# Performance work log

Hardware: AMD Instinct MI355X
Metric: run time of the kernel (lower is better)

Reference implementation:

```python
import jax, jax.numpy as jnp
import numpy as np

EPS = 1e-5
TOP_K = 3
W_THRESH = 0.01

def _bn(x, g, b):
    # training-mode batch norm over (N,H,W) per channel
    m = x.mean(axis=(0, 2, 3), keepdims=True)
    v = x.var(axis=(0, 2, 3), keepdims=True)
    return (x - m) * jax.lax.rsqrt(v + EPS) * g[None, :, None, None] + b[None, :, None, None]

def _conv(x, w, stride=1, pad=0, dil=1, groups=1):
    return jax.lax.conv_general_dilated(
        x, w, (stride, stride), [(pad, pad), (pad, pad)],
        rhs_dilation=(dil, dil),
        dimension_numbers=("NCHW", "OIHW", "NCHW"),
        feature_group_count=groups)

def _maxpool3(x):
    return jax.lax.reduce_window(x, -jnp.inf, jax.lax.max, (1, 1, 3, 3), (1, 1, 1, 1),
                                 [(0, 0), (0, 0), (1, 1), (1, 1)])

def _avgpool3(x):
    s = jax.lax.reduce_window(x, 0.0, jax.lax.add, (1, 1, 3, 3), (1, 1, 1, 1),
                              [(0, 0), (0, 0), (1, 1), (1, 1)])
    return s / 9.0  # count_include_pad=True as in torch avg_pool2d

def setup_inputs() -> dict:
    key = jax.random.key(0)
    ks = jax.random.split(key, 16)
    Cin, C = 128, 256
    B, H, W = 64, 32, 32
    f = lambda k, shp, s=0.05: jax.random.normal(k, shp, dtype=jnp.float32) * s
    gamma = lambda k, n: 1.0 + 0.1 * jax.random.normal(k, (n,), dtype=jnp.float32)
    return {
        "x": jax.random.normal(ks[0], (B, Cin, H, W), dtype=jnp.float32),
        "arch_weights": jax.random.normal(ks[1], (8,), dtype=jnp.float32),
        "w_in": f(ks[2], (C, Cin, 1, 1)),
        "g_in": gamma(ks[3], C), "b_in": jnp.zeros((C,), jnp.float32),
        "w3": f(ks[4], (C, C, 3, 3)),
        "g3": gamma(ks[5], C), "b3": jnp.zeros((C,), jnp.float32),
        "w5": f(ks[6], (C, C, 5, 5)),
        "g5": gamma(ks[7], C), "b5": jnp.zeros((C,), jnp.float32),
        "w_dw": f(ks[8], (C, 1, 3, 3), 0.2),
        "w_pw": f(ks[9], (C, C, 1, 1)),
        "gs": gamma(ks[10], C), "bs": jnp.zeros((C,), jnp.float32),
        "wd": f(ks[11], (C, C, 3, 3)),
        "gd": gamma(ks[12], C), "bd": jnp.zeros((C,), jnp.float32),
        "gmp": gamma(ks[13], C), "bmp": jnp.zeros((C,), jnp.float32),
        "gap": gamma(ks[14], C), "bap": jnp.zeros((C,), jnp.float32),
    }

def _forward(x, arch_weights, w_in, g_in, b_in, w3, g3, b3, w5, g5, b5,
             w_dw, w_pw, gs, bs, wd, gd, bd, gmp, bmp, gap, bap):
    # input transition: 1x1 conv -> BN -> ReLU (in_channels != out_channels)
    h = jax.nn.relu(_bn(_conv(x, w_in), g_in, b_in))
    # top-k thresholded renormalized mixture weights over 8 candidate ops
    w = jax.nn.softmax(arch_weights)
    tv, ti = jax.lax.top_k(w, TOP_K)
    sel = jnp.zeros_like(w).at[ti].set(tv)
    sel = jnp.where(sel >= W_THRESH, sel, 0.0)
    sel = sel / jnp.maximum(sel.sum(), 1e-12)
    r = jax.nn.relu(h)
    # op order: [none, max_pool_3x3, avg_pool_3x3, skip, conv_3x3, conv_5x5, sep_conv_3x3, dil_conv_3x3]
    out = sel[1] * _bn(_maxpool3(h), gmp, bmp)
    out = out + sel[2] * _bn(_avgpool3(h), gap, bap)
    out = out + sel[3] * h
    out = out + sel[4] * _bn(_conv(r, w3, pad=1), g3, b3)
    out = out + sel[5] * _bn(_conv(r, w5, pad=2), g5, b5)
    out = out + sel[6] * _bn(_conv(_conv(r, w_dw, pad=1, groups=r.shape[1]), w_pw), gs, bs)
    out = out + sel[7] * _bn(_conv(r, wd, pad=2, dil=2), gd, bd)
    return out

def reference(x, arch_weights, w_in, g_in, b_in, w3, g3, b3, w5, g5, b5,
              w_dw, w_pw, gs, bs, wd, gd, bd, gmp, bmp, gap, bap):
    return _forward(x, arch_weights, w_in, g_in, b_in, w3, g3, b3, w5, g5, b5,
                    w_dw, w_pw, gs, bs, wd, gd, bd, gmp, bmp, gap, bap)
```

## Files before the change

kernel.cpp:

```cpp
#include <hip/hip_runtime.h>

#define CIN_  128
#define C_    256
#define HW_   1024
#define NPC_  65536.0f
#define NB_   16384

constexpr size_t NELEM = 16777216ull;

__device__ float g_sel[8];
__device__ float g_stats[8 * 512];
__device__ int   g_isf32;
__device__ float g_h[NELEM];
__device__ float g_c3[NELEM];
__device__ float g_c5[NELEM];
__device__ float g_cd[NELEM];
__device__ float g_pm[NELEM];
__device__ float g_pa[NELEM];
__device__ float g_pw[NELEM];
__device__ float g_dw[NELEM];

__device__ float g_w5f[32 * 256 * 25 * 8];
__device__ float g_w3f[32 * 256 * 9 * 8];
__device__ float g_wdf[32 * 256 * 9 * 8];
__device__ float g_wtf[32 * 128 * 8];

__device__ __forceinline__ float u2f(unsigned short u) {
    union { unsigned int i; float f; } x; x.i = ((unsigned int)u) << 16; return x.f;
}
__device__ __forceinline__ unsigned short f2u(float f) {
    union { float f; unsigned int i; } x; x.f = f;
    unsigned int r = x.i + 0x7fffu + ((x.i >> 16) & 1u);
    return (unsigned short)(r >> 16);
}
__device__ __forceinline__ float ldq(const void* p, long i, int isf32) {
    return isf32 ? ((const float*)p)[i] : u2f(((const unsigned short*)p)[i]);
}

__global__ void k_prep(const void* __restrict__ x, const void* __restrict__ aw) {
    __shared__ int flag_s;
    __shared__ float red[256];
    const int t = threadIdx.x;
    for (int i = t; i < 8 * 512; i += 256) g_stats[i] = 0.f;
    const unsigned short* xu = (const unsigned short*)x;
    int bad = 0;
    for (int i = t; i < 8192; i += 256) {
        unsigned int e = (xu[i] >> 7) & 0xFFu;
        if (e >= 0xC6u) ++bad;
    }
    red[t] = (float)bad;
    __syncthreads();
    for (int off = 128; off > 0; off >>= 1) {
        if (t < off) red[t] += red[t + off];
        __syncthreads();
    }
    if (t == 0) { flag_s = (red[0] > 4.0f) ? 1 : 0; g_isf32 = flag_s; }
    __syncthreads();
    const int isf32 = flag_s;
    if (t == 0) {
        float w[8];
        float mx = -1e30f;
        for (int i = 0; i < 8; ++i) { w[i] = ldq(aw, i, isf32); mx = fmaxf(mx, w[i]); }
        float s = 0.f;
        for (int i = 0; i < 8; ++i) { w[i] = expf(w[i] - mx); s += w[i]; }
        for (int i = 0; i < 8; ++i) w[i] /= s;
        float sv[8] = {0,0,0,0,0,0,0,0};
        bool used[8] = {false,false,false,false,false,false,false,false};
        for (int k = 0; k < 3; ++k) {
            int bi = -1; float bv = -1.f;
            for (int i = 0; i < 8; ++i) if (!used[i] && w[i] > bv) { bv = w[i]; bi = i; }
            used[bi] = true; sv[bi] = bv;
        }
        float tot = 0.f;
        for (int i = 0; i < 8; ++i) { if (sv[i] < 0.01f) sv[i] = 0.f; tot += sv[i]; }
        tot = fmaxf(tot, 1e-12f);
        for (int i = 0; i < 8; ++i) g_sel[i] = sv[i] / tot;
    }
}

__global__ __launch_bounds__(256)
void k_wconv(const void* __restrict__ w3, const void* __restrict__ w5,
             const void* __restrict__ wd, const void* __restrict__ wi) {
    const int cg = blockIdx.x;
    const int t  = threadIdx.x;
    const int isf32 = g_isf32;
    for (int o = t; o < 51200; o += 256) {
        int u = o & 7, r = o >> 3, tap = r % 25, ci = r / 25;
        g_w5f[(size_t)cg * 51200 + o] =
            ldq(w5, ((long)(cg * 8 + u) * C_ + ci) * 25 + tap, isf32);
    }
    for (int o = t; o < 18432; o += 256) {
        int u = o & 7, r = o >> 3, tap = r % 9, ci = r / 9;
        long ii = ((long)(cg * 8 + u) * C_ + ci) * 9 + tap;
        g_w3f[(size_t)cg * 18432 + o] = ldq(w3, ii, isf32);
        g_wdf[(size_t)cg * 18432 + o] = ldq(wd, ii, isf32);
    }
    for (int o = t; o < 1024; o += 256) {
        int u = o & 7, ci = o >> 3;
        g_wtf[cg * 1024 + o] = ldq(wi, (long)(cg * 8 + u) * CIN_ + ci, isf32);
    }
}

__device__ __forceinline__ void stats_epilogue(float* red, float s, float s2,
                                               int t, int c, int slot) {
    __syncthreads();
    red[t] = s; red[t + 256] = s2;
    __syncthreads();
    for (int off = 128; off > 0; off >>= 1) {
        if (t < off) { red[t] += red[t + off]; red[t + 256] += red[t + 256 + off]; }
        __syncthreads();
    }
    if (t == 0) {
        atomicAdd(&g_stats[slot * 512 + c], red[0]);
        atomicAdd(&g_stats[slot * 512 + 256 + c], red[256]);
    }
}

__device__ __forceinline__ void stats_ep2(float* red, int t,
                                          float sA, float s2A, float sB, float s2B,
                                          int cA, int cB, int slot) {
    __syncthreads();
    red[t] = sA; red[t + 256] = s2A; red[t + 512] = sB; red[t + 768] = s2B;
    __syncthreads();
    for (int off = 128; off > 0; off >>= 1) {
        if (t < off) {
            red[t]       += red[t + off];
            red[t + 256] += red[t + 256 + off];
            red[t + 512] += red[t + 512 + off];
            red[t + 768] += red[t + 768 + off];
        }
        __syncthreads();
    }
    if (t == 0) {
        atomicAdd(&g_stats[slot * 512 + cA],       red[0]);
        atomicAdd(&g_stats[slot * 512 + 256 + cA], red[256]);
        atomicAdd(&g_stats[slot * 512 + cB],       red[512]);
        atomicAdd(&g_stats[slot * 512 + 256 + cB], red[768]);
    }
}

__global__ __launch_bounds__(256)
void k_trans(const void* __restrict__ xin) {
    __shared__ float xs[2][HW_];
    __shared__ float red[1024];
    const int t  = threadIdx.x;
    const int cg = blockIdx.x & 31;
    const int c0 = cg * 8;
    const int b  = blockIdx.x >> 5;
    const int isf32 = g_isf32;
    const float* wb = g_wtf + cg * 1024;
    float acc[8][4];
    #pragma unroll
    for (int k = 0; k < 8; ++k)
        #pragma unroll
        for (int j = 0; j < 4; ++j) acc[k][j] = 0.f;

    {
        size_t vi = (size_t)(b * CIN_) * 256 + t;
        float4 r0;
        if (isf32) r0 = ((const float4*)xin)[vi];
        else {
            ushort4 r = ((const ushort4*)xin)[vi];
            r0.x = u2f(r.x); r0.y = u2f(r.y); r0.z = u2f(r.z); r0.w = u2f(r.w);
        }
        xs[0][t*4+0] = r0.x; xs[0][t*4+1] = r0.y;
        xs[0][t*4+2] = r0.z; xs[0][t*4+3] = r0.w;
    }
    __syncthreads();
    int cur = 0;
    for (int ci = 0; ci < CIN_; ++ci) {
        float4 rN = {0.f, 0.f, 0.f, 0.f};
        if (ci + 1 < CIN_) {
            size_t vi = (size_t)(b * CIN_ + ci + 1) * 256 + t;
            if (isf32) rN = ((const float4*)xin)[vi];
            else {
                ushort4 r = ((const ushort4*)xin)[vi];
                rN.x = u2f(r.x); rN.y = u2f(r.y); rN.z = u2f(r.z); rN.w = u2f(r.w);
            }
        }
        const float x0v = xs[cur][t      ], x1v = xs[cur][t + 256];
        const float x2v = xs[cur][t + 512], x3v = xs[cur][t + 768];
        float4 wq0 = *(const float4*)(wb + ci * 8);
        float4 wq1 = *(const float4*)(wb + ci * 8 + 4);
        acc[0][0] += x0v*wq0.x; acc[0][1] += x1v*wq0.x; acc[0][2] += x2v*wq0.x; acc[0][3] += x3v*wq0.x;
        acc[1][0] += x0v*wq0.y; acc[1][1] += x1v*wq0.y; acc[1][2] += x2v*wq0.y; acc[1][3] += x3v*wq0.y;
        acc[2][0] += x0v*wq0.z; acc[2][1] += x1v*wq0.z; acc[2][2] += x2v*wq0.z; acc[2][3] += x3v*wq0.z;
        acc[3][0] += x0v*wq0.w; acc[3][1] += x1v*wq0.w; acc[3][2] += x2v*wq0.w; acc[3][3] += x3v*wq0.w;
        acc[4][0] += x0v*wq1.x; acc[4][1] += x1v*wq1.x; acc[4][2] += x2v*wq1.x; acc[4][3] += x3v*wq1.x;
        acc[5][0] += x0v*wq1.y; acc[5][1] += x1v*wq1.y; acc[5][2] += x2v*wq1.y; acc[5][3] += x3v*wq1.y;
        acc[6][0] += x0v*wq1.z; acc[6][1] += x1v*wq1.z; acc[6][2] += x2v*wq1.z; acc[6][3] += x3v*wq1.z;
        acc[7][0] += x0v*wq1.w; acc[7][1] += x1v*wq1.w; acc[7][2] += x2v*wq1.w; acc[7][3] += x3v*wq1.w;
        if (ci + 1 < CIN_) {
            float* xw = xs[cur ^ 1] + t * 4;
            xw[0] = rN.x; xw[1] = rN.y; xw[2] = rN.z; xw[3] = rN.w;
        }
        __syncthreads();
        cur ^= 1;
    }
    #pragma unroll
    for (int k = 0; k < 8; ++k) {
        float* o = g_dw + (size_t)(b * C_ + c0 + k) * HW_;
        o[t] = acc[k][0]; o[t + 256] = acc[k][1];
        o[t + 512] = acc[k][2]; o[t + 768] = acc[k][3];
    }
    #pragma unroll
    for (int k = 0; k < 8; k += 2) {
        float sA  = acc[k][0] + acc[k][1] + acc[k][2] + acc[k][3];
        float s2A = acc[k][0]*acc[k][0] + acc[k][1]*acc[k][1]
                  + acc[k][2]*acc[k][2] + acc[k][3]*acc[k][3];
        float sB  = acc[k+1][0] + acc[k+1][1] + acc[k+1][2] + acc[k+1][3];
        float s2B = acc[k+1][0]*acc[k+1][0] + acc[k+1][1]*acc[k+1][1]
                  + acc[k+1][2]*acc[k+1][2] + acc[k+1][3]*acc[k+1][3];
        stats_ep2(red, t, sA, s2A, sB, s2B, c0 + k, c0 + k + 1, 0);
    }
}

__global__ __launch_bounds__(256)
void k_bnrelu(const void* __restrict__ g, const void* __restrict__ bb) {
    size_t idx = ((size_t)blockIdx.x * 256 + threadIdx.x) * 4;
    int c = (int)((idx >> 10) & (C_ - 1));
    int isf32 = g_isf32;
    float mean = g_stats[c] * (1.0f / NPC_);
    float var  = g_stats[256 + c] * (1.0f / NPC_) - mean * mean;
    float rstd = rsqrtf(fmaxf(var, 0.f) + 1e-5f);
    float gv = ldq(g, c, isf32), bv = ldq(bb, c, isf32);
    float4 r = *(const float4*)(g_dw + idx);
    float4 h;
    h.x = fmaxf(0.f, (r.x - mean) * rstd * gv + bv);
    h.y = fmaxf(0.f, (r.y - mean) * rstd * gv + bv);
    h.z = fmaxf(0.f, (r.z - mean) * rstd * gv + bv);
    h.w = fmaxf(0.f, (r.w - mean) * rstd * gv + bv);
    *(float4*)(g_h + idx) = h;
}

__global__ __launch_bounds__(256)
void k_pool_fused() {
    const float s1 = g_sel[1], s2 = g_sel[2];
    if (s1 == 0.f && s2 == 0.f) return;
    __shared__ float xs[34 * 33];
    __shared__ float red[512];
    const int t = threadIdx.x;
    const int c = blockIdx.x & (C_ - 1);
    const int y  = t >> 3;
    const int x0 = (t & 7) * 4;
    const float* hp = g_h + (size_t)blockIdx.x * HW_;
    float4 r = *(const float4*)(hp + t * 4);
    float* xw = xs + y * 33 + x0;
    xw[0] = r.x; xw[1] = r.y; xw[2] = r.z; xw[3] = r.w;
    __syncthreads();
    float mx[4] = {0.f, 0.f, 0.f, 0.f};
    float sm[4] = {0.f, 0.f, 0.f, 0.f};
    #pragma unroll
    for (int ky = 0; ky < 3; ++ky) {
        int iy = y + ky - 1;
        if (iy < 0 || iy >= 32) continue;
        float row[6];
        #pragma unroll
        for (int i = 0; i < 6; ++i) {
            int ix = x0 + i - 1;
            row[i] = (ix >= 0 && ix < 32) ? xs[iy * 33 + ix] : 0.0f;
        }
        #pragma unroll
        for (int kx = 0; kx < 3; ++kx)
            #pragma unroll
            for (int j = 0; j < 4; ++j) {
                mx[j] = fmaxf(mx[j], row[j + kx]);
                sm[j] += row[j + kx];
            }
    }
    #pragma unroll
    for (int j = 0; j < 4; ++j) sm[j] *= (1.0f / 9.0f);
    const size_t ob = (size_t)blockIdx.x * HW_ + y * 32 + x0;
    if (s1 != 0.f) {
        float* o = g_pm + ob;
        o[0] = mx[0]; o[1] = mx[1]; o[2] = mx[2]; o[3] = mx[3];
        stats_epilogue(red, mx[0]+mx[1]+mx[2]+mx[3],
                       mx[0]*mx[0]+mx[1]*mx[1]+mx[2]*mx[2]+mx[3]*mx[3], t, c, 1);
    }
    if (s2 != 0.f) {
        float* o = g_pa + ob;
        o[0] = sm[0]; o[1] = sm[1]; o[2] = sm[2]; o[3] = sm[3];
        stats_epilogue(red, sm[0]+sm[1]+sm[2]+sm[3],
                       sm[0]*sm[0]+sm[1]*sm[1]+sm[2]*sm[2]+sm[3]*sm[3], t, c, 2);
    }
}

template<int KS, int DIL, int PAD, int SLOT>
__global__ __launch_bounds__(256)
void k_conv1() {
    if (g_sel[SLOT] == 0.0f) return;
    constexpr int TR   = 32 + 2 * PAD;
    constexpr int TAPS = KS * KS;
    __shared__ float xs[2][TR * 40];
    __shared__ float red[1024];
    const int t  = threadIdx.x;
    const int cg = blockIdx.x & 31;
    const int c0 = cg * 8;
    const int b  = blockIdx.x >> 5;
    const int y  = t >> 3;
    const int x0 = (t & 7) * 4;
    const float* hb = g_h + (size_t)b * C_ * HW_;
    const float* wb = (SLOT == 4 ? g_w3f : SLOT == 5 ? g_w5f : g_wdf)
                      + (size_t)cg * (C_ * TAPS * 8);
    float* obuf = (SLOT == 4) ? g_c3 : (SLOT == 5) ? g_c5 : g_cd;

    float acc[8][4];
    #pragma unroll
    for (int u = 0; u < 8; ++u)
        #pragma unroll
        for (int j = 0; j < 4; ++j) acc[u][j] = 0.f;

    {
        float* xf = &xs[0][0];
        for (int i = t; i < 2 * TR * 40; i += 256) xf[i] = 0.f;
    }
    __syncthreads();
    {
        float4 r0 = *(const float4*)(hb + t * 4);
        *(float4*)(xs[0] + (y + PAD) * 40 + 4 + x0) = r0;
    }
    __syncthreads();
    int cur = 0;

    for (int ci = 0; ci < C_; ++ci) {
        float4 rN = {0.f, 0.f, 0.f, 0.f};
        if (ci + 1 < C_)
            rN = *(const float4*)(hb + (size_t)(ci + 1) * HW_ + t * 4);
        const float* xsc = xs[cur];
        const float* wc  = wb + ci * (TAPS * 8);
        #pragma unroll
        for (int ky = 0; ky < KS; ++ky) {
            const int rr = (y + ky * DIL) * 40 + x0;
            float wnd[12];
            if (PAD == 1) {
                wnd[3] = xsc[rr + 3];
                float4 qb = *(const float4*)(xsc + rr + 4);
                wnd[4] = qb.x; wnd[5] = qb.y; wnd[6] = qb.z; wnd[7] = qb.w;
                wnd[8] = xsc[rr + 8];
            } else {
                float2 qa = *(const float2*)(xsc + rr + 2);
                float4 qb = *(const float4*)(xsc + rr + 4);
                float2 qc = *(const float2*)(xsc + rr + 8);
                wnd[2] = qa.x; wnd[3] = qa.y;
                wnd[4] = qb.x; wnd[5] = qb.y; wnd[6] = qb.z; wnd[7] = qb.w;
                wnd[8] = qc.x; wnd[9] = qc.y;
            }
            #pragma unroll
            for (int kx = 0; kx < KS; ++kx) {
                const float4 wA = *(const float4*)(wc + (ky * KS + kx) * 8);
                const float4 wB = *(const float4*)(wc + (ky * KS + kx) * 8 + 4);
                #pragma unroll
                for (int j = 0; j < 4; ++j) {
                    const float v = wnd[(4 - PAD) + j + kx * DIL];
                    acc[0][j] += v * wA.x; acc[1][j] += v * wA.y;
                    acc[2][j] += v * wA.z; acc[3][j] += v * wA.w;
                    acc[4][j] += v * wB.x; acc[5][j] += v * wB.y;
                    acc[6][j] += v * wB.z; acc[7][j] += v * wB.w;
                }
            }
        }
        if (ci + 1 < C_)
            *(float4*)(xs[cur ^ 1] + (y + PAD) * 40 + 4 + x0) = rN;
        __syncthreads();
        cur ^= 1;
    }

    #pragma unroll
    for (int u = 0; u < 8; ++u) {
        float4 o; o.x = acc[u][0]; o.y = acc[u][1]; o.z = acc[u][2]; o.w = acc[u][3];
        *(float4*)(obuf + (size_t)(b * C_ + c0 + u) * HW_ + y * 32 + x0) = o;
    }
    #pragma unroll
    for (int u = 0; u < 8; u += 2)
        stats_ep2(red, t,
            acc[u][0]+acc[u][1]+acc[u][2]+acc[u][3],
            acc[u][0]*acc[u][0]+acc[u][1]*acc[u][1]+acc[u][2]*acc[u][2]+acc[u][3]*acc[u][3],
            acc[u+1][0]+acc[u+1][1]+acc[u+1][2]+acc[u+1][3],
            acc[u+1][0]*acc[u+1][0]+acc[u+1][1]*acc[u+1][1]+acc[u+1][2]*acc[u+1][2]+acc[u+1][3]*acc[u+1][3],
            c0 + u, c0 + u + 1, SLOT);
}

__global__ __launch_bounds__(256)
void k_dw(const void* __restrict__ wt) {
    if (g_sel[6] == 0.0f) return;
    __shared__ float xs[34 * 33];
    const int t = threadIdx.x;
    const int c = blockIdx.x & (C_ - 1);
    const int y  = t >> 3;
    const int x0 = (t & 7) * 4;
    const int isf32 = g_isf32;
    const float* hp = g_h + (size_t)blockIdx.x * HW_;
    float4 r = *(const float4*)(hp + t * 4);
    float* xw = xs + y * 33 + x0;
    xw[0] = r.x; xw[1] = r.y; xw[2] = r.z; xw[3] = r.w;
    __syncthreads();
    float wv[9];
    #pragma unroll
    for (int k = 0; k < 9; ++k) wv[k] = ldq(wt, (long)c * 9 + k, isf32);
    float acc[4] = {0.f, 0.f, 0.f, 0.f};
    #pragma unroll
    for (int ky = 0; ky < 3; ++ky) {
        int iy = y + ky - 1;
        if (iy < 0 || iy >= 32) continue;
        float row[6];
        #pragma unroll
        for (int i = 0; i < 6; ++i) {
            int ix = x0 + i - 1;
            row[i] = (ix >= 0 && ix < 32) ? xs[iy * 33 + ix] : 0.0f;
        }
        #pragma unroll
        for (int kx = 0; kx < 3; ++kx)
            #pragma unroll
            for (int j = 0; j < 4; ++j)
                acc[j] += row[j + kx] * wv[ky * 3 + kx];
    }
    float* o = g_dw + (size_t)blockIdx.x * HW_ + y * 32 + x0;
    o[0] = acc[0]; o[1] = acc[1]; o[2] = acc[2]; o[3] = acc[3];
}

__global__ __launch_bounds__(256)
void k_pw(const void* __restrict__ wt) {
    if (g_sel[6] == 0.0f) return;
    __shared__ float xs[HW_];
    __shared__ float red[1024];
    const int t = threadIdx.x;
    const int c0 = (blockIdx.x & 31) * 8;
    const int b  = blockIdx.x >> 5;
    const int isf32 = g_isf32;
    const float* hb = g_dw + (size_t)b * C_ * HW_;
    float acc[8][4];
    #pragma unroll
    for (int k = 0; k < 8; ++k)
        #pragma unroll
        for (int j = 0; j < 4; ++j) acc[k][j] = 0.f;
    for (int ci = 0; ci < C_; ++ci) {
        __syncthreads();
        float4 r = *(const float4*)(hb + (size_t)ci * HW_ + t * 4);
        xs[t*4+0] = r.x; xs[t*4+1] = r.y; xs[t*4+2] = r.z; xs[t*4+3] = r.w;
        __syncthreads();
        const float x0v = xs[t], x1v = xs[t + 256], x2v = xs[t + 512], x3v = xs[t + 768];
        #pragma unroll
        for (int k = 0; k < 8; ++k) {
            float wv = ldq(wt, (long)(c0 + k) * C_ + ci, isf32);
            acc[k][0] += x0v * wv; acc[k][1] += x1v * wv;
            acc[k][2] += x2v * wv; acc[k][3] += x3v * wv;
        }
    }
    #pragma unroll
    for (int k = 0; k < 8; ++k) {
        float* o = g_pw + (size_t)(b * C_ + c0 + k) * HW_;
        o[t] = acc[k][0]; o[t + 256] = acc[k][1];
        o[t + 512] = acc[k][2]; o[t + 768] = acc[k][3];
    }
    #pragma unroll
    for (int k = 0; k < 8; k += 2) {
        float sA  = acc[k][0] + acc[k][1] + acc[k][2] + acc[k][3];
        float s2A = acc[k][0]*acc[k][0] + acc[k][1]*acc[k][1]
                  + acc[k][2]*acc[k][2] + acc[k][3]*acc[k][3];
        float sB  = acc[k+1][0] + acc[k+1][1] + acc[k+1][2] + acc[k+1][3];
        float s2B = acc[k+1][0]*acc[k+1][0] + acc[k+1][1]*acc[k+1][1]
                  + acc[k+1][2]*acc[k+1][2] + acc[k+1][3]*acc[k+1][3];
        stats_ep2(red, t, sA, s2A, sB, s2B, c0 + k, c0 + k + 1, 6);
    }
}

__device__ __forceinline__ void bn_term(float4& o, const float* buf, size_t idx,
                                        int c, int slot, float sv,
                                        const void* g, const void* bb, int isf32) {
    float mean = g_stats[slot * 512 + c] * (1.0f / NPC_);
    float var  = g_stats[slot * 512 + 256 + c] * (1.0f / NPC_) - mean * mean;
    float rstd = rsqrtf(fmaxf(var, 0.f) + 1e-5f);
    float gv = ldq(g, c, isf32), bv = ldq(bb, c, isf32);
    float4 r = *(const float4*)(buf + idx);
    o.x += sv * ((r.x - mean) * rstd * gv + bv);
    o.y += sv * ((r.y - mean) * rstd * gv + bv);
    o.z += sv * ((r.z - mean) * rstd * gv + bv);
    o.w += sv * ((r.w - mean) * rstd * gv + bv);
}

__global__ __launch_bounds__(256)
void k_final_all(void* __restrict__ out,
                 const void* __restrict__ gmp, const void* __restrict__ bmp,
                 const void* __restrict__ gap, const void* __restrict__ bap,
                 const void* __restrict__ g3,  const void* __restrict__ b3,
                 const void* __restrict__ g5,  const void* __restrict__ b5,
                 const void* __restrict__ gs,  const void* __restrict__ bs,
                 const void* __restrict__ gd,  const void* __restrict__ bd) {
    size_t idx = ((size_t)blockIdx.x * 256 + threadIdx.x) * 4;
    int c = (int)((idx >> 10) & (C_ - 1));
    int isf32 = g_isf32;
    float4 o = {0.f, 0.f, 0.f, 0.f};
    float s3 = g_sel[3];
    if (s3 != 0.f) {
        float4 h = *(const float4*)(g_h + idx);
        o.x = s3 * h.x; o.y = s3 * h.y; o.z = s3 * h.z; o.w = s3 * h.w;
    }
    float sv;
    if ((sv = g_sel[1]) != 0.f) bn_term(o, g_pm, idx, c, 1, sv, gmp, bmp, isf32);
    if ((sv = g_sel[2]) != 0.f) bn_term(o, g_pa, idx, c, 2, sv, gap, bap, isf32);
    if ((sv = g_sel[4]) != 0.f) bn_term(o, g_c3, idx, c, 4, sv, g3,  b3,  isf32);
    if ((sv = g_sel[5]) != 0.f) bn_term(o, g_c5, idx, c, 5, sv, g5,  b5,  isf32);
    if ((sv = g_sel[6]) != 0.f) bn_term(o, g_pw, idx, c, 6, sv, gs,  bs,  isf32);
    if ((sv = g_sel[7]) != 0.f) bn_term(o, g_cd, idx, c, 7, sv, gd,  bd,  isf32);
    if (isf32) {
        *(float4*)((float*)out + idx) = o;
    } else {
        ushort4 u; u.x = f2u(o.x); u.y = f2u(o.y); u.z = f2u(o.z); u.w = f2u(o.w);
        *(ushort4*)((unsigned short*)out + idx) = u;
    }
}

extern "C" void kernel_launch(void* const* d_in, const int* in_sizes, int n_in,
                              void* d_out, int out_size, void* d_ws, size_t ws_size,
                              hipStream_t stream) {
    const void* x    = d_in[0];
    const void* aw   = d_in[1];
    const void* w_in = d_in[2];
    const void* g_in = d_in[3];
    const void* b_in = d_in[4];
    const void* w3   = d_in[5];
    const void* g3   = d_in[6];
    const void* b3   = d_in[7];
    const void* w5   = d_in[8];
    const void* g5   = d_in[9];
    const void* b5   = d_in[10];
    const void* wdw  = d_in[11];
    const void* wpw  = d_in[12];
    const void* gs   = d_in[13];
    const void* bs   = d_in[14];
    const void* wd   = d_in[15];
    const void* gd   = d_in[16];
    const void* bd   = d_in[17];
    const void* gmp  = d_in[18];
    const void* bmp  = d_in[19];
    const void* gap  = d_in[20];
    const void* bap  = d_in[21];

    dim3 Bk(256);
    dim3 Gfull(NB_);
    dim3 Gc8(2048);

    k_prep<<<dim3(1), Bk, 0, stream>>>(x, aw);
    k_wconv<<<dim3(32), Bk, 0, stream>>>(w3, w5, wd, w_in);

    k_trans<<<Gc8, Bk, 0, stream>>>(x);
    k_bnrelu<<<Gfull, Bk, 0, stream>>>(g_in, b_in);

    k_pool_fused<<<Gfull, Bk, 0, stream>>>();

    k_conv1<3, 1, 1, 4><<<Gc8, Bk, 0, stream>>>();
    k_conv1<5, 1, 2, 5><<<Gc8, Bk, 0, stream>>>();
    k_conv1<3, 2, 2, 7><<<Gc8, Bk, 0, stream>>>();

    k_dw<<<Gfull, Bk, 0, stream>>>(wdw);
    k_pw<<<Gc8, Bk, 0, stream>>>(wpw);

    k_final_all<<<Gfull, Bk, 0, stream>>>(d_out,
        gmp, bmp, gap, bap, g3, b3, g5, b5, gs, bs, gd, bd);
}
```

Before: 1.219 ms.

## Make conv tiles per-wavefront and drop block barriers in 1x1 convs

The spatial conv kernels now give each 64-lane wavefront its own 8-row tile with its own double-buffered shared-memory halo. This removes the per-input-channel __syncthreads, at the cost of redundant halo loads and larger per-block LDS. The 1x1 input and pointwise convs read activations straight from global memory instead of staging through shared memory with barriers. The pointwise weights are pre-transposed into a channel-interleaved float buffer for vectorized loads. Stats reduction is factored into a helper.

```diff
diff --git a/kernel.cpp b/kernel.cpp
--- a/kernel.cpp
+++ b/kernel.cpp
@@ -24,6 +24,7 @@
 __device__ float g_w3f[32 * 256 * 9 * 8];
 __device__ float g_wdf[32 * 256 * 9 * 8];
 __device__ float g_wtf[32 * 128 * 8];
+__device__ float g_wpf[32 * 256 * 8];
 
 __device__ __forceinline__ float u2f(unsigned short u) {
     union { unsigned int i; float f; } x; x.i = ((unsigned int)u) << 16; return x.f;
@@ -36,6 +37,16 @@
 __device__ __forceinline__ float ldq(const void* p, long i, int isf32) {
     return isf32 ? ((const float*)p)[i] : u2f(((const unsigned short*)p)[i]);
 }
+
+#define FMA8X4(acc, wq0, wq1, x0v, x1v, x2v, x3v)                                     \
+    acc[0][0] += x0v*wq0.x; acc[0][1] += x1v*wq0.x; acc[0][2] += x2v*wq0.x; acc[0][3] += x3v*wq0.x; \
+    acc[1][0] += x0v*wq0.y; acc[1][1] += x1v*wq0.y; acc[1][2] += x2v*wq0.y; acc[1][3] += x3v*wq0.y; \
+    acc[2][0] += x0v*wq0.z; acc[2][1] += x1v*wq0.z; acc[2][2] += x2v*wq0.z; acc[2][3] += x3v*wq0.z; \
+    acc[3][0] += x0v*wq0.w; acc[3][1] += x1v*wq0.w; acc[3][2] += x2v*wq0.w; acc[3][3] += x3v*wq0.w; \
+    acc[4][0] += x0v*wq1.x; acc[4][1] += x1v*wq1.x; acc[4][2] += x2v*wq1.x; acc[4][3] += x3v*wq1.x; \
+    acc[5][0] += x0v*wq1.y; acc[5][1] += x1v*wq1.y; acc[5][2] += x2v*wq1.y; acc[5][3] += x3v*wq1.y; \
+    acc[6][0] += x0v*wq1.z; acc[6][1] += x1v*wq1.z; acc[6][2] += x2v*wq1.z; acc[6][3] += x3v*wq1.z; \
+    acc[7][0] += x0v*wq1.w; acc[7][1] += x1v*wq1.w; acc[7][2] += x2v*wq1.w; acc[7][3] += x3v*wq1.w;
 
 __global__ void k_prep(const void* __restrict__ x, const void* __restrict__ aw) {
     __shared__ int flag_s;
@@ -80,7 +91,8 @@
 
 __global__ __launch_bounds__(256)
 void k_wconv(const void* __restrict__ w3, const void* __restrict__ w5,
-             const void* __restrict__ wd, const void* __restrict__ wi) {
+             const void* __restrict__ wd, const void* __restrict__ wi,
+             const void* __restrict__ wp) {
     const int cg = blockIdx.x;
     const int t  = threadIdx.x;
     const int isf32 = g_isf32;
@@ -99,6 +111,10 @@
         int u = o & 7, ci = o >> 3;
         g_wtf[cg * 1024 + o] = ldq(wi, (long)(cg * 8 + u) * CIN_ + ci, isf32);
     }
+    for (int o = t; o < 2048; o += 256) {
+        int u = o & 7, ci = o >> 3;
+        g_wpf[cg * 2048 + o] = ldq(wp, (long)(cg * 8 + u) * C_ + ci, isf32);
+    }
 }
 
 __device__ __forceinline__ void stats_epilogue(float* red, float s, float s2,
@@ -139,15 +155,25 @@
     }
 }
 
+__device__ __forceinline__ void stats_all8(float* red, int t, float acc[8][4],
+                                           int c0, int slot) {
+    #pragma unroll
+    for (int u = 0; u < 8; u += 2)
+        stats_ep2(red, t,
+            acc[u][0]+acc[u][1]+acc[u][2]+acc[u][3],
+            acc[u][0]*acc[u][0]+acc[u][1]*acc[u][1]+acc[u][2]*acc[u][2]+acc[u][3]*acc[u][3],
+            acc[u+1][0]+acc[u+1][1]+acc[u+1][2]+acc[u+1][3],
+            acc[u+1][0]*acc[u+1][0]+acc[u+1][1]*acc[u+1][1]+acc[u+1][2]*acc[u+1][2]+acc[u+1][3]*acc[u+1][3],
+            c0 + u, c0 + u + 1, slot);
+}
+
 __global__ __launch_bounds__(256)
 void k_trans(const void* __restrict__ xin) {
-    __shared__ float xs[2][HW_];
     __shared__ float red[1024];
     const int t  = threadIdx.x;
     const int cg = blockIdx.x & 31;
     const int c0 = cg * 8;
     const int b  = blockIdx.x >> 5;
-    const int isf32 = g_isf32;
     const float* wb = g_wtf + cg * 1024;
     float acc[8][4];
     #pragma unroll
@@ -155,47 +181,26 @@
         #pragma unroll
         for (int j = 0; j < 4; ++j) acc[k][j] = 0.f;
 
-    {
-        size_t vi = (size_t)(b * CIN_) * 256 + t;
-        float4 r0;
-        if (isf32) r0 = ((const float4*)xin)[vi];
-        else {
-            ushort4 r = ((const ushort4*)xin)[vi];
-            r0.x = u2f(r.x); r0.y = u2f(r.y); r0.z = u2f(r.z); r0.w = u2f(r.w);
-        }
-        xs[0][t*4+0] = r0.x; xs[0][t*4+1] = r0.y;
-        xs[0][t*4+2] = r0.z; xs[0][t*4+3] = r0.w;
-    }
-    __syncthreads();
-    int cur = 0;
-    for (int ci = 0; ci < CIN_; ++ci) {
-        float4 rN = {0.f, 0.f, 0.f, 0.f};
-        if (ci + 1 < CIN_) {
-            size_t vi = (size_t)(b * CIN_ + ci + 1) * 256 + t;
-            if (isf32) rN = ((const float4*)xin)[vi];
-            else {
-                ushort4 r = ((const ushort4*)xin)[vi];
-                rN.x = u2f(r.x); rN.y = u2f(r.y); rN.z = u2f(r.z); rN.w = u2f(r.w);
-            }
-        }
-        const float x0v = xs[cur][t      ], x1v = xs[cur][t + 256];
-        const float x2v = xs[cur][t + 512], x3v = xs[cur][t + 768];
-        float4 wq0 = *(const float4*)(wb + ci * 8);
-        float4 wq1 = *(const float4*)(wb + ci * 8 + 4);
-        acc[0][0] += x0v*wq0.x; acc[0][1] += x1v*wq0.x; acc[0][2] += x2v*wq0.x; acc[0][3] += x3v*wq0.x;
-        acc[1][0] += x0v*wq0.y; acc[1][1] += x1v*wq0.y; acc[1][2] += x2v*wq0.y; acc[1][3] += x3v*wq0.y;
-        acc[2][0] += x0v*wq0.z; acc[2][1] += x1v*wq0.z; acc[2][2] += x2v*wq0.z; acc[2][3] += x3v*wq0.z;
-        acc[3][0] += x0v*wq0.w; acc[3][1] += x1v*wq0.w; acc[3][2] += x2v*wq0.w; acc[3][3] += x3v*wq0.w;
-        acc[4][0] += x0v*wq1.x; acc[4][1] += x1v*wq1.x; acc[4][2] += x2v*wq1.x; acc[4][3] += x3v*wq1.x;
-        acc[5][0] += x0v*wq1.y; acc[5][1] += x1v*wq1.y; acc[5][2] += x2v*wq1.y; acc[5][3] += x3v*wq1.y;
-        acc[6][0] += x0v*wq1.z; acc[6][1] += x1v*wq1.z; acc[6][2] += x2v*wq1.z; acc[6][3] += x3v*wq1.z;
-        acc[7][0] += x0v*wq1.w; acc[7][1] += x1v*wq1.w; acc[7][2] += x2v*wq1.w; acc[7][3] += x3v*wq1.w;
-        if (ci + 1 < CIN_) {
-            float* xw = xs[cur ^ 1] + t * 4;
-            xw[0] = rN.x; xw[1] = rN.y; xw[2] = rN.z; xw[3] = rN.w;
-        }
-        __syncthreads();
-        cur ^= 1;
+    const size_t base0 = (size_t)b * CIN_ * 1024 + t;
+    if (g_isf32) {
+        const float* xf = (const float*)xin;
+        for (int ci = 0; ci < CIN_; ++ci) {
+            const float* xp = xf + base0 + (size_t)ci * 1024;
+            float x0v = xp[0], x1v = xp[256], x2v = xp[512], x3v = xp[768];
+            float4 wq0 = *(const float4*)(wb + ci * 8);
+            float4 wq1 = *(const float4*)(wb + ci * 8 + 4);
+            FMA8X4(acc, wq0, wq1, x0v, x1v, x2v, x3v)
+        }
+    } else {
+        const unsigned short* xu = (const unsigned short*)xin;
+        for (int ci = 0; ci < CIN_; ++ci) {
+            const unsigned short* xp = xu + base0 + (size_t)ci * 1024;
+            float x0v = u2f(xp[0]),   x1v = u2f(xp[256]);
+            float x2v = u2f(xp[512]), x3v = u2f(xp[768]);
+            float4 wq0 = *(const float4*)(wb + ci * 8);
+            float4 wq1 = *(const float4*)(wb + ci * 8 + 4);
+            FMA8X4(acc, wq0, wq1, x0v, x1v, x2v, x3v)
+        }
     }
     #pragma unroll
     for (int k = 0; k < 8; ++k) {
@@ -203,16 +208,7 @@
         o[t] = acc[k][0]; o[t + 256] = acc[k][1];
         o[t + 512] = acc[k][2]; o[t + 768] = acc[k][3];
     }
-    #pragma unroll
-    for (int k = 0; k < 8; k += 2) {
-        float sA  = acc[k][0] + acc[k][1] + acc[k][2] + acc[k][3];
-        float s2A = acc[k][0]*acc[k][0] + acc[k][1]*acc[k][1]
-                  + acc[k][2]*acc[k][2] + acc[k][3]*acc[k][3];
-        float sB  = acc[k+1][0] + acc[k+1][1] + acc[k+1][2] + acc[k+1][3];
-        float s2B = acc[k+1][0]*acc[k+1][0] + acc[k+1][1]*acc[k+1][1]
-                  + acc[k+1][2]*acc[k+1][2] + acc[k+1][3]*acc[k+1][3];
-        stats_ep2(red, t, sA, s2A, sB, s2B, c0 + k, c0 + k + 1, 0);
-    }
+    stats_all8(red, t, acc, c0, 0);
 }
 
 __global__ __launch_bounds__(256)
@@ -289,21 +285,28 @@
 __global__ __launch_bounds__(256)
 void k_conv1() {
     if (g_sel[SLOT] == 0.0f) return;
-    constexpr int TR   = 32 + 2 * PAD;
+    constexpr int TRW  = 8 + 2 * PAD;
     constexpr int TAPS = KS * KS;
-    __shared__ float xs[2][TR * 40];
-    __shared__ float red[1024];
+    __shared__ float xs[4][2][TRW * 40];
     const int t  = threadIdx.x;
+    const int w  = t >> 6;
+    const int l  = t & 63;
     const int cg = blockIdx.x & 31;
     const int c0 = cg * 8;
     const int b  = blockIdx.x >> 5;
-    const int y  = t >> 3;
-    const int x0 = (t & 7) * 4;
+    const int y  = l >> 3;
+    const int x0 = (l & 7) * 4;
+    const int y0 = w * 8;
     const float* hb = g_h + (size_t)b * C_ * HW_;
     const float* wb = (SLOT == 4 ? g_w3f : SLOT == 5 ? g_w5f : g_wdf)
                       + (size_t)cg * (C_ * TAPS * 8);
     float* obuf = (SLOT == 4) ? g_c3 : (SLOT == 5) ? g_c5 : g_cd;
 
+    const int grA = y0 - PAD + y;
+    const bool okA = (grA >= 0) && (grA < 32);
+    const int grB = grA + 8;
+    const bool okB = (y < 2 * PAD) && (grB < 32);
+
     float acc[8][4];
     #pragma unroll
     for (int u = 0; u < 8; ++u)
@@ -311,22 +314,23 @@
         for (int j = 0; j < 4; ++j) acc[u][j] = 0.f;
 
     {
-        float* xf = &xs[0][0];
-        for (int i = t; i < 2 * TR * 40; i += 256) xf[i] = 0.f;
-    }
-    __syncthreads();
-    {
-        float4 r0 = *(const float4*)(hb + t * 4);
-        *(float4*)(xs[0] + (y + PAD) * 40 + 4 + x0) = r0;
-    }
-    __syncthreads();
+        float* xw = &xs[w][0][0];
+        for (int i = l; i < 2 * TRW * 40; i += 64) xw[i] = 0.f;
+    }
+    if (okA) *(float4*)(&xs[w][0][y * 40 + 4 + x0]) =
+        *(const float4*)(hb + (size_t)grA * 32 + x0);
+    if (okB) *(float4*)(&xs[w][0][(y + 8) * 40 + 4 + x0]) =
+        *(const float4*)(hb + (size_t)grB * 32 + x0);
     int cur = 0;
 
     for (int ci = 0; ci < C_; ++ci) {
-        float4 rN = {0.f, 0.f, 0.f, 0.f};
-        if (ci + 1 < C_)
-            rN = *(const float4*)(hb + (size_t)(ci + 1) * HW_ + t * 4);
-        const float* xsc = xs[cur];
+        float4 rA = {0.f,0.f,0.f,0.f}, rB = {0.f,0.f,0.f,0.f};
+        if (ci + 1 < C_) {
+            const float* hn = hb + (size_t)(ci + 1) * HW_;
+            if (okA) rA = *(const float4*)(hn + grA * 32 + x0);
+            if (okB) rB = *(const float4*)(hn + grB * 32 + x0);
+        }
+        const float* xsc = xs[w][cur];
         const float* wc  = wb + ci * (TAPS * 8);
         #pragma unroll
         for (int ky = 0; ky < KS; ++ky) {
@@ -359,25 +363,21 @@
                 }
             }
         }
-        if (ci + 1 < C_)
-            *(float4*)(xs[cur ^ 1] + (y + PAD) * 40 + 4 + x0) = rN;
-        __syncthreads();
+        if (ci + 1 < C_) {
+            float* xn = xs[w][cur ^ 1];
+            if (okA) *(float4*)(xn + y * 40 + 4 + x0) = rA;
+            if (okB) *(float4*)(xn + (y + 8) * 40 + 4 + x0) = rB;
+        }
         cur ^= 1;
     }
 
     #pragma unroll
     for (int u = 0; u < 8; ++u) {
         float4 o; o.x = acc[u][0]; o.y = acc[u][1]; o.z = acc[u][2]; o.w = acc[u][3];
-        *(float4*)(obuf + (size_t)(b * C_ + c0 + u) * HW_ + y * 32 + x0) = o;
-    }
-    #pragma unroll
-    for (int u = 0; u < 8; u += 2)
-        stats_ep2(red, t,
-            acc[u][0]+acc[u][1]+acc[u][2]+acc[u][3],
-            acc[u][0]*acc[u][0]+acc[u][1]*acc[u][1]+acc[u][2]*acc[u][2]+acc[u][3]*acc[u][3],
-            acc[u+1][0]+acc[u+1][1]+acc[u+1][2]+acc[u+1][3],
-            acc[u+1][0]*acc[u+1][0]+acc[u+1][1]*acc[u+1][1]+acc[u+1][2]*acc[u+1][2]+acc[u+1][3]*acc[u+1][3],
-            c0 + u, c0 + u + 1, SLOT);
+        *(float4*)(obuf + (size_t)(b * C_ + c0 + u) * HW_ + (y0 + y) * 32 + x0) = o;
+    }
+    float* red = &xs[0][0][0];
+    stats_all8(red, t, acc, c0, SLOT);
 }
 
 __global__ __launch_bounds__(256)
@@ -419,32 +419,26 @@
 }
 
 __global__ __launch_bounds__(256)
-void k_pw(const void* __restrict__ wt) {
+void k_pw() {
     if (g_sel[6] == 0.0f) return;
-    __shared__ float xs[HW_];
     __shared__ float red[1024];
-    const int t = threadIdx.x;
-    const int c0 = (blockIdx.x & 31) * 8;
+    const int t  = threadIdx.x;
+    const int cg = blockIdx.x & 31;
+    const int c0 = cg * 8;
     const int b  = blockIdx.x >> 5;
-    const int isf32 = g_isf32;
-    const float* hb = g_dw + (size_t)b * C_ * HW_;
+    const float* hb = g_dw + (size_t)b * C_ * HW_ + t;
+    const float* wb = g_wpf + cg * 2048;
     float acc[8][4];
     #pragma unroll
     for (int k = 0; k < 8; ++k)
         #pragma unroll
         for (int j = 0; j < 4; ++j) acc[k][j] = 0.f;
     for (int ci = 0; ci < C_; ++ci) {
-        __syncthreads();
-        float4 r = *(const float4*)(hb + (size_t)ci * HW_ + t * 4);
-        xs[t*4+0] = r.x; xs[t*4+1] = r.y; xs[t*4+2] = r.z; xs[t*4+3] = r.w;
-        __syncthreads();
-        const float x0v = xs[t], x1v = xs[t + 256], x2v = xs[t + 512], x3v = xs[t + 768];
-        #pragma unroll
-        for (int k = 0; k < 8; ++k) {
-            float wv = ldq(wt, (long)(c0 + k) * C_ + ci, isf32);
-            acc[k][0] += x0v * wv; acc[k][1] += x1v * wv;
-            acc[k][2] += x2v * wv; acc[k][3] += x3v * wv;
-        }
+        const float* hp = hb + (size_t)ci * HW_;
+        float x0v = hp[0], x1v = hp[256], x2v = hp[512], x3v = hp[768];
+        float4 wq0 = *(const float4*)(wb + ci * 8);
+        float4 wq1 = *(const float4*)(wb + ci * 8 + 4);
+        FMA8X4(acc, wq0, wq1, x0v, x1v, x2v, x3v)
     }
     #pragma unroll
     for (int k = 0; k < 8; ++k) {
@@ -452,16 +446,7 @@
         o[t] = acc[k][0]; o[t + 256] = acc[k][1];
         o[t + 512] = acc[k][2]; o[t + 768] = acc[k][3];
     }
-    #pragma unroll
-    for (int k = 0; k < 8; k += 2) {
-        float sA  = acc[k][0] + acc[k][1] + acc[k][2] + acc[k][3];
-        float s2A = acc[k][0]*acc[k][0] + acc[k][1]*acc[k][1]
-                  + acc[k][2]*acc[k][2] + acc[k][3]*acc[k][3];
-        float sB  = acc[k+1][0] + acc[k+1][1] + acc[k+1][2] + acc[k+1][3];
-        float s2B = acc[k+1][0]*acc[k+1][0] + acc[k+1][1]*acc[k+1][1]
-                  + acc[k+1][2]*acc[k+1][2] + acc[k+1][3]*acc[k+1][3];
-        stats_ep2(red, t, sA, s2A, sB, s2B, c0 + k, c0 + k + 1, 6);
-    }
+    stats_all8(red, t, acc, c0, 6);
 }
 
 __device__ __forceinline__ void bn_term(float4& o, const float* buf, size_t idx,
@@ -541,7 +526,7 @@
     dim3 Gc8(2048);
 
     k_prep<<<dim3(1), Bk, 0, stream>>>(x, aw);
-    k_wconv<<<dim3(32), Bk, 0, stream>>>(w3, w5, wd, w_in);
+    k_wconv<<<dim3(32), Bk, 0, stream>>>(w3, w5, wd, w_in, wpw);
 
     k_trans<<<Gc8, Bk, 0, stream>>>(x);
     k_bnrelu<<<Gfull, Bk, 0, stream>>>(g_in, b_in);
@@ -553,7 +538,7 @@
     k_conv1<3, 2, 2, 7><<<Gc8, Bk, 0, stream>>>();
 
     k_dw<<<Gfull, Bk, 0, stream>>>(wdw);
-    k_pw<<<Gc8, Bk, 0, stream>>>(wpw);
+    k_pw<<<Gc8, Bk, 0, stream>>>();
 
     k_final_all<<<Gfull, Bk, 0, stream>>>(d_out,
         gmp, bmp, gap, bap, g3, b3, g5, b5, gs, bs, gd, bd);
```

Measured after the change: 1.216 ms. No clear change (-0.2%).
